# Kernel optimization log

Hardware: AMD Instinct MI355X
Metric: run time of the kernel (lower is better)

The kernel has to match this reference:

```python
import jax, jax.numpy as jnp
import numpy as np

SCALE = 0.125  # 1/sqrt(d_head)
QLEN, KLEN, BSZ, NHEAD, DHEAD = 1024, 1024, 4, 16, 64
RLEN = KLEN + 1


def rel_shift(x, klen):
    # x: [q, r, b, n] -> relative shift -> [q, klen, b, n]
    q, r, b, n = x.shape
    x = x.reshape(r, q, b, n)[1:]
    x = x.reshape(q, r - 1, b, n)[:, :klen]
    return x


def setup_inputs() -> dict:
    key = jax.random.key(0)
    ks = jax.random.split(key, 9)
    q_head = jax.random.normal(ks[0], (QLEN, BSZ, NHEAD, DHEAD), jnp.float32)
    k_head_h = jax.random.normal(ks[1], (KLEN, BSZ, NHEAD, DHEAD), jnp.float32)
    v_head_h = jax.random.normal(ks[2], (KLEN, BSZ, NHEAD, DHEAD), jnp.float32)
    k_head_r = jax.random.normal(ks[3], (RLEN, BSZ, NHEAD, DHEAD), jnp.float32)
    seg_embed = jax.random.normal(ks[4], (2, NHEAD, DHEAD), jnp.float32)
    seg_mat = jax.random.randint(ks[5], (QLEN, KLEN, BSZ), 0, 2) > 0  # bool
    r_w_bias = jax.random.normal(ks[6], (NHEAD, DHEAD), jnp.float32) * 0.02
    r_r_bias = jax.random.normal(ks[7], (NHEAD, DHEAD), jnp.float32) * 0.02
    r_s_bias = jax.random.normal(ks[8], (NHEAD, DHEAD), jnp.float32) * 0.02
    # causal mask: 1.0 where key position j is after query position i
    i = jnp.arange(QLEN)[:, None]
    j = jnp.arange(KLEN)[None, :]
    attn_mask = (j > i).astype(jnp.float32).reshape(QLEN, KLEN, 1, 1)
    return {
        "q_head": q_head, "k_head_h": k_head_h, "v_head_h": v_head_h,
        "k_head_r": k_head_r, "seg_embed": seg_embed, "seg_mat": seg_mat,
        "r_w_bias": r_w_bias, "r_r_bias": r_r_bias, "r_s_bias": r_s_bias,
        "attn_mask": attn_mask,
    }


def reference(q_head, k_head_h, v_head_h, k_head_r, seg_embed, seg_mat,
              r_w_bias, r_r_bias, r_s_bias, attn_mask):
    # content-based score: [q, k, b, n]
    ac = jnp.einsum('ibnd,jbnd->ijbn', q_head + r_w_bias, k_head_h)
    # position-based score, then relative shift
    bd = jnp.einsum('ibnd,jbnd->ijbn', q_head + r_r_bias, k_head_r)
    bd = rel_shift(bd, klen=ac.shape[1])
    # segment-based score: [q, 2, b, n] -> select same/diff per (i,j,b)
    ef = jnp.einsum('ibnd,snd->isbn', q_head + r_s_bias, seg_embed)
    ef = jnp.where(seg_mat[..., None], ef[:, 1:2], ef[:, 0:1])  # [q,k,b,n]
    attn_score = (ac + bd + ef) * SCALE
    attn_score = attn_score - 1e30 * attn_mask
    attn_prob = jax.nn.softmax(attn_score, axis=1)  # softmax over key axis j
    attn_vec = jnp.einsum('ijbn,jbnd->ibnd', attn_prob, v_head_h)
    return attn_vec
```

## Files before the change

### kernel.cpp

```cpp
#include <hip/hip_runtime.h>

#define QLEN  1024
#define KLEN  1024
#define BSZ   4
#define NHEAD 16
#define DHEAD 64
#define PS    4096
#define SCALE 0.125f
#define MSHIFT 16.0f

#define WK 72
#define WR 72
#define WV 68
#define WP 68

typedef __attribute__((ext_vector_type(8))) short  short8;
typedef __attribute__((ext_vector_type(4))) short  short4v;
typedef __attribute__((ext_vector_type(4))) float  float4v;

union S8 { short8 v; short4v h[2]; unsigned short u[8]; };

__device__ __forceinline__ unsigned short f2b(float f) {
    unsigned u; __builtin_memcpy(&u, &f, 4);
    return (unsigned short)((u + 0x8000u) >> 16);
}
__device__ __forceinline__ float b2f(unsigned short s) {
    unsigned u = ((unsigned)s) << 16;
    float f; __builtin_memcpy(&f, &u, 4);
    return f;
}

#define MFMA(a,b,c) __builtin_amdgcn_mfma_f32_16x16x32_bf16((a),(b),(c),0,0,0)

__global__ __launch_bounds__(256)
void seg_pack(const int* __restrict__ sm, unsigned long long* __restrict__ bits)
{
    int gw = (blockIdx.x << 2) + (threadIdx.x >> 6);
    int jw = gw & 15;
    int ib = gw >> 4;
    int b  = ib & 3;
    int i  = ib >> 2;
    int jj = threadIdx.x & 63;
    int v  = sm[(i*KLEN + (jw << 6) + jj)*BSZ + b];
    unsigned long long m = __ballot(v != 0);
    if (jj == 0) bits[gw] = m;
}

__global__ __launch_bounds__(256, 3)
void relattn_mfma7(const float* __restrict__ q,
                   const float* __restrict__ kh,
                   const float* __restrict__ vh,
                   const float* __restrict__ kr,
                   const float* __restrict__ seg_embed,
                   const unsigned long long* __restrict__ segbits,
                   const float* __restrict__ rw,
                   const float* __restrict__ rr,
                   const float* __restrict__ rs,
                   float* __restrict__ out)
{
    __shared__ __align__(16) unsigned short sK [64*WK];
    __shared__ __align__(16) unsigned short sKr[128*WR];
    __shared__ __align__(16) unsigned short sVt[64*WV];
    __shared__ __align__(16) unsigned short sBD[64*WP];

    const int tid  = threadIdx.x;
    const int lane = tid & 63;
    const int wave = tid >> 6;
    const int quad = lane >> 4;
    const int l16  = lane & 15;
    const int bx   = blockIdx.x;
    const int h    = blockIdx.y;
    const int b    = h >> 4;
    const int n    = h & 15;
    const int qt   = (b & 1) ? bx : (15 - bx);
    const int i0   = qt << 6;
    const int m0   = wave << 4;
    const int hoff = h << 6;
    const int d0   = quad << 3;
    const int G0   = 961 - i0;
    const int srow = tid >> 4;
    const int c4   = (tid & 15) << 2;

    float4 pK[4], pV[4], pR[4];
    {
        float4 pR2[4];
        const float4 zf4 = make_float4(0.f, 0.f, 0.f, 0.f);
        #pragma unroll
        for (int k2 = 0; k2 < 4; ++k2) {
            int row = srow + (k2 << 4);
            pK[k2] = *(const float4*)(kh + row*PS + hoff + c4);
            pV[k2] = *(const float4*)(vh + row*PS + hoff + c4);
            int g1 = G0 + row;
            pR[k2]  = (g1 <= 1024) ? *(const float4*)(kr + g1*PS + hoff + c4) : zf4;
            int g2 = G0 + 64 + row;
            pR2[k2] = (g2 <= 1024) ? *(const float4*)(kr + g2*PS + hoff + c4) : zf4;
        }

        float qv[16], rwv[16], rrv[16], rsv[16];
        {
            const float* qp = q + (i0 + m0 + l16)*PS + hoff;
            *(float4*)&qv[0]  = *(const float4*)(qp + d0);
            *(float4*)&qv[4]  = *(const float4*)(qp + d0 + 4);
            *(float4*)&qv[8]  = *(const float4*)(qp + 32 + d0);
            *(float4*)&qv[12] = *(const float4*)(qp + 32 + d0 + 4);
            const float* rwp = rw + n*DHEAD;
            *(float4*)&rwv[0]  = *(const float4*)(rwp + d0);
            *(float4*)&rwv[4]  = *(const float4*)(rwp + d0 + 4);
            *(float4*)&rwv[8]  = *(const float4*)(rwp + 32 + d0);
            *(float4*)&rwv[12] = *(const float4*)(rwp + 32 + d0 + 4);
            const float* rrp = rr + n*DHEAD;
            *(float4*)&rrv[0]  = *(const float4*)(rrp + d0);
            *(float4*)&rrv[4]  = *(const float4*)(rrp + d0 + 4);
            *(float4*)&rrv[8]  = *(const float4*)(rrp + 32 + d0);
            *(float4*)&rrv[12] = *(const float4*)(rrp + 32 + d0 + 4);
            const float* rsp = rs + n*DHEAD;
            *(float4*)&rsv[0]  = *(const float4*)(rsp + d0);
            *(float4*)&rsv[4]  = *(const float4*)(rsp + d0 + 4);
            *(float4*)&rsv[8]  = *(const float4*)(rsp + 32 + d0);
            *(float4*)&rsv[12] = *(const float4*)(rsp + 32 + d0 + 4);
        }
        S8 aw0_, aw1_, ar0_, ar1_;
        #pragma unroll
        for (int m = 0; m < 8; ++m) {
            aw0_.u[m] = f2b(qv[m]   + rwv[m]);
            aw1_.u[m] = f2b(qv[8+m] + rwv[8+m]);
            ar0_.u[m] = f2b(qv[m]   + rrv[m]);
            ar1_.u[m] = f2b(qv[8+m] + rrv[8+m]);
        }
        float ef0r_[4], ef1r_[4];
        {
            const float* se0 = seg_embed + n*DHEAD;
            const float* se1 = seg_embed + (NHEAD + n)*DHEAD;
            float e0 = 0.f, e1 = 0.f;
            #pragma unroll
            for (int m = 0; m < 8; ++m) {
                float qs = qv[m] + rsv[m];
                e0 += qs * se0[d0 + m];  e1 += qs * se1[d0 + m];
                float qs2 = qv[8+m] + rsv[8+m];
                e0 += qs2 * se0[32 + d0 + m];  e1 += qs2 * se1[32 + d0 + m];
            }
            e0 += __shfl_xor(e0, 16); e0 += __shfl_xor(e0, 32);
            e1 += __shfl_xor(e1, 16); e1 += __shfl_xor(e1, 32);
            #pragma unroll
            for (int r = 0; r < 4; ++r) {
                ef0r_[r] = __shfl(e0, (quad << 2) + r);
                ef1r_[r] = __shfl(e1, (quad << 2) + r);
            }
        }

        #pragma unroll
        for (int k2 = 0; k2 < 4; ++k2) {
            int row = srow + (k2 << 4);
            float4 kv = pK[k2];
            short4v kb = {(short)f2b(kv.x),(short)f2b(kv.y),(short)f2b(kv.z),(short)f2b(kv.w)};
            *(short4v*)&sK[row*WK + c4] = kb;
            float4 vv = pV[k2];
            sVt[(c4+0)*WV + row] = f2b(vv.x);
            sVt[(c4+1)*WV + row] = f2b(vv.y);
            sVt[(c4+2)*WV + row] = f2b(vv.z);
            sVt[(c4+3)*WV + row] = f2b(vv.w);
            float4 r1 = pR[k2];
            short4v rb1 = {(short)f2b(r1.x),(short)f2b(r1.y),(short)f2b(r1.z),(short)f2b(r1.w)};
            *(short4v*)&sKr[row*WR + c4] = rb1;
            float4 r2 = pR2[k2];
            short4v rb2 = {(short)f2b(r2.x),(short)f2b(r2.y),(short)f2b(r2.z),(short)f2b(r2.w)};
            *(short4v*)&sKr[(64 + row)*WR + c4] = rb2;
        }

        sK[0] = sK[0];
        __syncthreads();

        #pragma unroll
        for (int m = 0; m < 8; ++m) {  }
        float lp[4];
        float4v Ov[4];
        #pragma unroll
        for (int r = 0; r < 4; ++r) lp[r] = 0.f;
        #pragma unroll
        for (int cb = 0; cb < 4; ++cb) Ov[cb] = (float4v){0.f,0.f,0.f,0.f};

        for (int jt = 0; jt <= qt; ++jt) {
            const int  j0   = jt << 6;
            const bool diag = (jt == qt);
            const bool more = (jt < qt);
            const int  rot  = (jt & 1) << 2;

            if (more) {
                const int j0n = j0 + 64;
                const float4 zf4l = make_float4(0.f, 0.f, 0.f, 0.f);
                #pragma unroll
                for (int k2 = 0; k2 < 4; ++k2) {
                    int row = srow + (k2 << 4);
                    pK[k2] = *(const float4*)(kh + (j0n + row)*PS + hoff + c4);
                    pV[k2] = *(const float4*)(vh + (j0n + row)*PS + hoff + c4);
                    int g = G0 + ((jt + 2) << 6) + row;
                    pR[k2] = (g <= 1024) ? *(const float4*)(kr + g*PS + hoff + c4) : zf4l;
                }
            }
            unsigned long long wbits[4];
            #pragma unroll
            for (int r = 0; r < 4; ++r) {
                int il = m0 + (quad << 2) + r;
                wbits[r] = segbits[(((i0+il) << 2) + b)*16 + jt] >> l16;
            }

            const int bbHi = diag ? wave : 3;
            float4v ac[4];
            #pragma unroll
            for (int bb = 0; bb < 4; ++bb) {
                ac[bb] = (float4v){0.f,0.f,0.f,0.f};
                if (bb <= bbHi) {
                    const unsigned short* kp = &sK[((bb<<4) + l16)*WK + d0];
                    short8 b0 = *(const short8*)kp;
                    short8 b1 = *(const short8*)(kp + 32);
                    ac[bb] = MFMA(aw0_.v, b0, ac[bb]);
                    ac[bb] = MFMA(aw1_.v, b1, ac[bb]);
                }
            }

            const int cbLo = 3 - wave;
            const int cbHi = diag ? 3 : (7 - wave);
            #pragma unroll
            for (int cb = 0; cb < 8; ++cb) {
                if (cb >= cbLo && cb <= cbHi) {
                    const unsigned short* rp = &sKr[((((cb + rot) & 7) << 4) + l16)*WR + d0];
                    short8 b0 = *(const short8*)rp;
                    short8 b1 = *(const short8*)(rp + 32);
                    float4v z = (float4v){0.f,0.f,0.f,0.f};
                    z = MFMA(ar0_.v, b0, z);
                    z = MFMA(ar1_.v, b1, z);
                    #pragma unroll
                    for (int r = 0; r < 4; ++r) {
                        int il = m0 + (quad << 2) + r;
                        int jl = (cb << 4) + l16 - 63 + il;
                        if (jl >= 0 && jl < 64)
                            sBD[il*WP + jl] = f2b(z[r]);
                    }
                }
            }

            #pragma unroll
            for (int r = 0; r < 4; ++r) {
                const int il = m0 + (quad << 2) + r;
                float psum = 0.f;
                #pragma unroll
                for (int bb = 0; bb < 4; ++bb) {
                    const int jl = (bb << 4) + l16;
                    float bd = b2f(sBD[il*WP + jl]);
                    float ef = ((wbits[r] >> (bb << 4)) & 1ull) ? ef1r_[r] : ef0r_[r];
                    float s  = (ac[bb][r] + bd + ef) * SCALE - MSHIFT;
                    if (j0 + jl > i0 + il) s = -1e30f;
                    float p = __expf(s);
                    psum += p;
                    sBD[il*WP + jl] = f2b(p);
                }
                lp[r] += psum;
            }

            {
                const unsigned short* pr = &sBD[(m0 + l16)*WP + d0];
                S8 pa0, pa1;
                pa0.h[0] = *(const short4v*)pr;
                pa0.h[1] = *(const short4v*)(pr + 4);
                pa1.h[0] = *(const short4v*)(pr + 32);
                pa1.h[1] = *(const short4v*)(pr + 36);
                const bool k2on = !(diag && wave < 2);
                #pragma unroll
                for (int cb = 0; cb < 4; ++cb) {
                    const unsigned short* vp = &sVt[((cb<<4) + l16)*WV + d0];
                    S8 v0, v1;
                    v0.h[0] = *(const short4v*)vp;
                    v0.h[1] = *(const short4v*)(vp + 4);
                    Ov[cb] = MFMA(pa0.v, v0.v, Ov[cb]);
                    if (k2on) {
                        v1.h[0] = *(const short4v*)(vp + 32);
                        v1.h[1] = *(const short4v*)(vp + 36);
                        Ov[cb] = MFMA(pa1.v, v1.v, Ov[cb]);
                    }
                }
            }

            if (more) {
                __syncthreads();
                const int krslot = (jt & 1) << 6;
                #pragma unroll
                for (int k2 = 0; k2 < 4; ++k2) {
                    int row = srow + (k2 << 4);
                    float4 kv = pK[k2];
                    short4v kb = {(short)f2b(kv.x),(short)f2b(kv.y),(short)f2b(kv.z),(short)f2b(kv.w)};
                    *(short4v*)&sK[row*WK + c4] = kb;
                    float4 vv = pV[k2];
                    sVt[(c4+0)*WV + row] = f2b(vv.x);
                    sVt[(c4+1)*WV + row] = f2b(vv.y);
                    sVt[(c4+2)*WV + row] = f2b(vv.z);
                    sVt[(c4+3)*WV + row] = f2b(vv.w);
                    float4 rv = pR[k2];
                    short4v rb = {(short)f2b(rv.x),(short)f2b(rv.y),(short)f2b(rv.z),(short)f2b(rv.w)};
                    *(short4v*)&sKr[(krslot + row)*WR + c4] = rb;
                }
                __syncthreads();
            }
        }

        #pragma unroll
        for (int r = 0; r < 4; ++r) {
            float l = lp[r];
            l += __shfl_xor(l, 1);
            l += __shfl_xor(l, 2);
            l += __shfl_xor(l, 4);
            l += __shfl_xor(l, 8);
            const float inv = 1.f / l;
            const int il = m0 + (quad << 2) + r;
            #pragma unroll
            for (int cb = 0; cb < 4; ++cb)
                out[(i0+il)*PS + hoff + (cb<<4) + l16] = Ov[cb][r] * inv;
        }
    }
}

extern "C" void kernel_launch(void* const* d_in, const int* in_sizes, int n_in,
                              void* d_out, int out_size, void* d_ws, size_t ws_size,
                              hipStream_t stream)
{
    const float* q  = (const float*)d_in[0];
    const float* kh = (const float*)d_in[1];
    const float* vh = (const float*)d_in[2];
    const float* kr = (const float*)d_in[3];
    const float* se = (const float*)d_in[4];
    const int*   sm = (const int*)  d_in[5];
    const float* rw = (const float*)d_in[6];
    const float* rr = (const float*)d_in[7];
    const float* rs = (const float*)d_in[8];
    float* o = (float*)d_out;
    unsigned long long* bits = (unsigned long long*)d_ws;
    (void)in_sizes; (void)n_in; (void)out_size; (void)ws_size;

    seg_pack<<<dim3(QLEN*BSZ*16/4), 256, 0, stream>>>(sm, bits);

    dim3 grid(QLEN/64, BSZ*NHEAD);
    relattn_mfma7<<<grid, 256, 0, stream>>>(q, kh, vh, kr, se, bits, rw, rr, rs, o);
}
```

Measured before the change: 287.4 us.

## Swizzle LDS tiles, vectorize seg packing, reorder blocks, raise occupancy

Replaces the padded shared-memory layouts with XOR-swizzled unpadded tiles, which shrinks LDS per block so the launch bound can rise to four blocks per SM while still avoiding bank conflicts. The segment-packing kernel now reads int4 across the batch dimension and emits four ballots per wave, cutting its thread count and load instructions. The attention kernel moves to a 1D grid with a new causal-tile ordering meant to balance long and short query tiles across the machine. It also adds s_setprio around the MFMA sections. Raising the occupancy target may cause register spills.

```diff
diff --git a/kernel.cpp b/kernel.cpp
--- a/kernel.cpp
+++ b/kernel.cpp
@@ -9,11 +9,6 @@
 #define SCALE 0.125f
 #define MSHIFT 16.0f
 
-#define WK 72
-#define WR 72
-#define WV 68
-#define WP 68
-
 typedef __attribute__((ext_vector_type(8))) short  short8;
 typedef __attribute__((ext_vector_type(4))) short  short4v;
 typedef __attribute__((ext_vector_type(4))) float  float4v;
@@ -30,24 +25,31 @@
     return f;
 }
 
+__device__ __forceinline__ int swz (int row, int col) { return (row << 6) + (col ^ (( row        & 7) << 3)); }
+__device__ __forceinline__ int swzV(int row, int col) { return (row << 6) + (col ^ (((row >> 2) & 7) << 3)); }
+
 #define MFMA(a,b,c) __builtin_amdgcn_mfma_f32_16x16x32_bf16((a),(b),(c),0,0,0)
 
 __global__ __launch_bounds__(256)
-void seg_pack(const int* __restrict__ sm, unsigned long long* __restrict__ bits)
+void seg_pack(const int4* __restrict__ sm4, unsigned long long* __restrict__ bits)
 {
-    int gw = (blockIdx.x << 2) + (threadIdx.x >> 6);
-    int jw = gw & 15;
-    int ib = gw >> 4;
-    int b  = ib & 3;
-    int i  = ib >> 2;
+    int w  = (blockIdx.x << 2) + (threadIdx.x >> 6);
+    int i  = w >> 4;
+    int jw = w & 15;
     int jj = threadIdx.x & 63;
-    int v  = sm[(i*KLEN + (jw << 6) + jj)*BSZ + b];
-    unsigned long long m = __ballot(v != 0);
-    if (jj == 0) bits[gw] = m;
-}
-
-__global__ __launch_bounds__(256, 3)
-void relattn_mfma7(const float* __restrict__ q,
+    int4 v = sm4[i*KLEN + (jw << 6) + jj];
+    unsigned long long m0 = __ballot(v.x != 0);
+    unsigned long long m1 = __ballot(v.y != 0);
+    unsigned long long m2 = __ballot(v.z != 0);
+    unsigned long long m3 = __ballot(v.w != 0);
+    if (jj == 0) {
+        unsigned long long* p = bits + (i << 6) + jw;
+        p[0] = m0; p[16] = m1; p[32] = m2; p[48] = m3;
+    }
+}
+
+__global__ __launch_bounds__(256, 4)
+void relattn_mfma8(const float* __restrict__ q,
                    const float* __restrict__ kh,
                    const float* __restrict__ vh,
                    const float* __restrict__ kr,
@@ -58,21 +60,26 @@
                    const float* __restrict__ rs,
                    float* __restrict__ out)
 {
-    __shared__ __align__(16) unsigned short sK [64*WK];
-    __shared__ __align__(16) unsigned short sKr[128*WR];
-    __shared__ __align__(16) unsigned short sVt[64*WV];
-    __shared__ __align__(16) unsigned short sBD[64*WP];
+    __shared__ __align__(16) unsigned short sK [ 64*64];
+    __shared__ __align__(16) unsigned short sKr[128*64];
+    __shared__ __align__(16) unsigned short sVt[ 64*64];
+    __shared__ __align__(16) unsigned short sBD[ 64*64];
 
     const int tid  = threadIdx.x;
     const int lane = tid & 63;
     const int wave = tid >> 6;
     const int quad = lane >> 4;
     const int l16  = lane & 15;
-    const int bx   = blockIdx.x;
-    const int h    = blockIdx.y;
+
+    const int id = blockIdx.x;
+    const int h  = id & 63;
+    const int t  = id >> 6;
+    const int m  = t & 3;
+    const int kq = t >> 2;
+    const int qt = (kq == 0) ? m : (kq == 1) ? (15 - m) : (kq == 2) ? (m + 4) : (11 - m);
+
     const int b    = h >> 4;
     const int n    = h & 15;
-    const int qt   = (b & 1) ? bx : (15 - bx);
     const int i0   = qt << 6;
     const int m0   = wave << 4;
     const int hoff = h << 6;
@@ -81,9 +88,8 @@
     const int srow = tid >> 4;
     const int c4   = (tid & 15) << 2;
 
-    float4 pK[4], pV[4], pR[4];
+    float4 pK[4], pV[4], pR[4], pR2[4];
     {
-        float4 pR2[4];
         const float4 zf4 = make_float4(0.f, 0.f, 0.f, 0.f);
         #pragma unroll
         for (int k2 = 0; k2 < 4; ++k2) {
@@ -95,226 +101,226 @@
             int g2 = G0 + 64 + row;
             pR2[k2] = (g2 <= 1024) ? *(const float4*)(kr + g2*PS + hoff + c4) : zf4;
         }
-
-        float qv[16], rwv[16], rrv[16], rsv[16];
-        {
-            const float* qp = q + (i0 + m0 + l16)*PS + hoff;
-            *(float4*)&qv[0]  = *(const float4*)(qp + d0);
-            *(float4*)&qv[4]  = *(const float4*)(qp + d0 + 4);
-            *(float4*)&qv[8]  = *(const float4*)(qp + 32 + d0);
-            *(float4*)&qv[12] = *(const float4*)(qp + 32 + d0 + 4);
-            const float* rwp = rw + n*DHEAD;
-            *(float4*)&rwv[0]  = *(const float4*)(rwp + d0);
-            *(float4*)&rwv[4]  = *(const float4*)(rwp + d0 + 4);
-            *(float4*)&rwv[8]  = *(const float4*)(rwp + 32 + d0);
-            *(float4*)&rwv[12] = *(const float4*)(rwp + 32 + d0 + 4);
-            const float* rrp = rr + n*DHEAD;
-            *(float4*)&rrv[0]  = *(const float4*)(rrp + d0);
-            *(float4*)&rrv[4]  = *(const float4*)(rrp + d0 + 4);
-            *(float4*)&rrv[8]  = *(const float4*)(rrp + 32 + d0);
-            *(float4*)&rrv[12] = *(const float4*)(rrp + 32 + d0 + 4);
-            const float* rsp = rs + n*DHEAD;
-            *(float4*)&rsv[0]  = *(const float4*)(rsp + d0);
-            *(float4*)&rsv[4]  = *(const float4*)(rsp + d0 + 4);
-            *(float4*)&rsv[8]  = *(const float4*)(rsp + 32 + d0);
-            *(float4*)&rsv[12] = *(const float4*)(rsp + 32 + d0 + 4);
-        }
-        S8 aw0_, aw1_, ar0_, ar1_;
-        #pragma unroll
-        for (int m = 0; m < 8; ++m) {
-            aw0_.u[m] = f2b(qv[m]   + rwv[m]);
-            aw1_.u[m] = f2b(qv[8+m] + rwv[8+m]);
-            ar0_.u[m] = f2b(qv[m]   + rrv[m]);
-            ar1_.u[m] = f2b(qv[8+m] + rrv[8+m]);
-        }
-        float ef0r_[4], ef1r_[4];
-        {
-            const float* se0 = seg_embed + n*DHEAD;
-            const float* se1 = seg_embed + (NHEAD + n)*DHEAD;
-            float e0 = 0.f, e1 = 0.f;
+    }
+
+    float qv[16], rwv[16], rrv[16], rsv[16];
+    {
+        const float* qp = q + (i0 + m0 + l16)*PS + hoff;
+        *(float4*)&qv[0]  = *(const float4*)(qp + d0);
+        *(float4*)&qv[4]  = *(const float4*)(qp + d0 + 4);
+        *(float4*)&qv[8]  = *(const float4*)(qp + 32 + d0);
+        *(float4*)&qv[12] = *(const float4*)(qp + 32 + d0 + 4);
+        const float* rwp = rw + n*DHEAD;
+        *(float4*)&rwv[0]  = *(const float4*)(rwp + d0);
+        *(float4*)&rwv[4]  = *(const float4*)(rwp + d0 + 4);
+        *(float4*)&rwv[8]  = *(const float4*)(rwp + 32 + d0);
+        *(float4*)&rwv[12] = *(const float4*)(rwp + 32 + d0 + 4);
+        const float* rrp = rr + n*DHEAD;
+        *(float4*)&rrv[0]  = *(const float4*)(rrp + d0);
+        *(float4*)&rrv[4]  = *(const float4*)(rrp + d0 + 4);
+        *(float4*)&rrv[8]  = *(const float4*)(rrp + 32 + d0);
+        *(float4*)&rrv[12] = *(const float4*)(rrp + 32 + d0 + 4);
+        const float* rsp = rs + n*DHEAD;
+        *(float4*)&rsv[0]  = *(const float4*)(rsp + d0);
+        *(float4*)&rsv[4]  = *(const float4*)(rsp + d0 + 4);
+        *(float4*)&rsv[8]  = *(const float4*)(rsp + 32 + d0);
+        *(float4*)&rsv[12] = *(const float4*)(rsp + 32 + d0 + 4);
+    }
+    S8 aw0, aw1, ar0, ar1;
+    #pragma unroll
+    for (int mm = 0; mm < 8; ++mm) {
+        aw0.u[mm] = f2b(qv[mm]   + rwv[mm]);
+        aw1.u[mm] = f2b(qv[8+mm] + rwv[8+mm]);
+        ar0.u[mm] = f2b(qv[mm]   + rrv[mm]);
+        ar1.u[mm] = f2b(qv[8+mm] + rrv[8+mm]);
+    }
+    float ef0r[4], ef1r[4];
+    {
+        const float* se0 = seg_embed + n*DHEAD;
+        const float* se1 = seg_embed + (NHEAD + n)*DHEAD;
+        float e0 = 0.f, e1 = 0.f;
+        #pragma unroll
+        for (int mm = 0; mm < 8; ++mm) {
+            float qs = qv[mm] + rsv[mm];
+            e0 += qs * se0[d0 + mm];  e1 += qs * se1[d0 + mm];
+            float qs2 = qv[8+mm] + rsv[8+mm];
+            e0 += qs2 * se0[32 + d0 + mm];  e1 += qs2 * se1[32 + d0 + mm];
+        }
+        e0 += __shfl_xor(e0, 16); e0 += __shfl_xor(e0, 32);
+        e1 += __shfl_xor(e1, 16); e1 += __shfl_xor(e1, 32);
+        #pragma unroll
+        for (int r = 0; r < 4; ++r) {
+            ef0r[r] = __shfl(e0, (quad << 2) + r);
+            ef1r[r] = __shfl(e1, (quad << 2) + r);
+        }
+    }
+
+    #pragma unroll
+    for (int k2 = 0; k2 < 4; ++k2) {
+        int row = srow + (k2 << 4);
+        float4 kv = pK[k2];
+        short4v kb = {(short)f2b(kv.x),(short)f2b(kv.y),(short)f2b(kv.z),(short)f2b(kv.w)};
+        *(short4v*)&sK[swz(row, c4)] = kb;
+        float4 vv = pV[k2];
+        sVt[swzV(c4+0, row)] = f2b(vv.x);
+        sVt[swzV(c4+1, row)] = f2b(vv.y);
+        sVt[swzV(c4+2, row)] = f2b(vv.z);
+        sVt[swzV(c4+3, row)] = f2b(vv.w);
+        float4 r1 = pR[k2];
+        short4v rb1 = {(short)f2b(r1.x),(short)f2b(r1.y),(short)f2b(r1.z),(short)f2b(r1.w)};
+        *(short4v*)&sKr[swz(row, c4)] = rb1;
+        float4 r2 = pR2[k2];
+        short4v rb2 = {(short)f2b(r2.x),(short)f2b(r2.y),(short)f2b(r2.z),(short)f2b(r2.w)};
+        *(short4v*)&sKr[swz(64 + row, c4)] = rb2;
+    }
+    __syncthreads();
+
+    float lp[4];
+    float4v Ov[4];
+    #pragma unroll
+    for (int r = 0; r < 4; ++r) lp[r] = 0.f;
+    #pragma unroll
+    for (int cb = 0; cb < 4; ++cb) Ov[cb] = (float4v){0.f,0.f,0.f,0.f};
+
+    for (int jt = 0; jt <= qt; ++jt) {
+        const int  j0   = jt << 6;
+        const bool diag = (jt == qt);
+        const bool more = (jt < qt);
+        const int  rot  = (jt & 1) << 2;
+
+        if (more) {
+            const int j0n = j0 + 64;
+            const float4 zf4l = make_float4(0.f, 0.f, 0.f, 0.f);
             #pragma unroll
-            for (int m = 0; m < 8; ++m) {
-                float qs = qv[m] + rsv[m];
-                e0 += qs * se0[d0 + m];  e1 += qs * se1[d0 + m];
-                float qs2 = qv[8+m] + rsv[8+m];
-                e0 += qs2 * se0[32 + d0 + m];  e1 += qs2 * se1[32 + d0 + m];
-            }
-            e0 += __shfl_xor(e0, 16); e0 += __shfl_xor(e0, 32);
-            e1 += __shfl_xor(e1, 16); e1 += __shfl_xor(e1, 32);
-            #pragma unroll
-            for (int r = 0; r < 4; ++r) {
-                ef0r_[r] = __shfl(e0, (quad << 2) + r);
-                ef1r_[r] = __shfl(e1, (quad << 2) + r);
-            }
-        }
-
-        #pragma unroll
-        for (int k2 = 0; k2 < 4; ++k2) {
-            int row = srow + (k2 << 4);
-            float4 kv = pK[k2];
-            short4v kb = {(short)f2b(kv.x),(short)f2b(kv.y),(short)f2b(kv.z),(short)f2b(kv.w)};
-            *(short4v*)&sK[row*WK + c4] = kb;
-            float4 vv = pV[k2];
-            sVt[(c4+0)*WV + row] = f2b(vv.x);
-            sVt[(c4+1)*WV + row] = f2b(vv.y);
-            sVt[(c4+2)*WV + row] = f2b(vv.z);
-            sVt[(c4+3)*WV + row] = f2b(vv.w);
-            float4 r1 = pR[k2];
-            short4v rb1 = {(short)f2b(r1.x),(short)f2b(r1.y),(short)f2b(r1.z),(short)f2b(r1.w)};
-            *(short4v*)&sKr[row*WR + c4] = rb1;
-            float4 r2 = pR2[k2];
-            short4v rb2 = {(short)f2b(r2.x),(short)f2b(r2.y),(short)f2b(r2.z),(short)f2b(r2.w)};
-            *(short4v*)&sKr[(64 + row)*WR + c4] = rb2;
-        }
-
-        sK[0] = sK[0];
-        __syncthreads();
-
-        #pragma unroll
-        for (int m = 0; m < 8; ++m) {  }
-        float lp[4];
-        float4v Ov[4];
-        #pragma unroll
-        for (int r = 0; r < 4; ++r) lp[r] = 0.f;
-        #pragma unroll
-        for (int cb = 0; cb < 4; ++cb) Ov[cb] = (float4v){0.f,0.f,0.f,0.f};
-
-        for (int jt = 0; jt <= qt; ++jt) {
-            const int  j0   = jt << 6;
-            const bool diag = (jt == qt);
-            const bool more = (jt < qt);
-            const int  rot  = (jt & 1) << 2;
-
-            if (more) {
-                const int j0n = j0 + 64;
-                const float4 zf4l = make_float4(0.f, 0.f, 0.f, 0.f);
+            for (int k2 = 0; k2 < 4; ++k2) {
+                int row = srow + (k2 << 4);
+                pK[k2] = *(const float4*)(kh + (j0n + row)*PS + hoff + c4);
+                pV[k2] = *(const float4*)(vh + (j0n + row)*PS + hoff + c4);
+                int g = G0 + ((jt + 2) << 6) + row;
+                pR[k2] = (g <= 1024) ? *(const float4*)(kr + g*PS + hoff + c4) : zf4l;
+            }
+        }
+        unsigned long long wbits[4];
+        #pragma unroll
+        for (int r = 0; r < 4; ++r) {
+            int il = m0 + (quad << 2) + r;
+            wbits[r] = segbits[(((i0+il) << 2) + b)*16 + jt] >> l16;
+        }
+
+        __builtin_amdgcn_s_setprio(1);
+        const int bbHi = diag ? wave : 3;
+        float4v ac[4];
+        #pragma unroll
+        for (int bb = 0; bb < 4; ++bb) {
+            ac[bb] = (float4v){0.f,0.f,0.f,0.f};
+            if (bb <= bbHi) {
+                const int krow = (bb << 4) + l16;
+                short8 b0 = *(const short8*)&sK[swz(krow, d0)];
+                short8 b1 = *(const short8*)&sK[swz(krow, d0 + 32)];
+                ac[bb] = MFMA(aw0.v, b0, ac[bb]);
+                ac[bb] = MFMA(aw1.v, b1, ac[bb]);
+            }
+        }
+
+        const int cbLo = 3 - wave;
+        const int cbHi = diag ? 3 : (7 - wave);
+        #pragma unroll
+        for (int cb = 0; cb < 8; ++cb) {
+            if (cb >= cbLo && cb <= cbHi) {
+                const int rrow = (((cb + rot) & 7) << 4) + l16;
+                short8 b0 = *(const short8*)&sKr[swz(rrow, d0)];
+                short8 b1 = *(const short8*)&sKr[swz(rrow, d0 + 32)];
+                float4v z = (float4v){0.f,0.f,0.f,0.f};
+                z = MFMA(ar0.v, b0, z);
+                z = MFMA(ar1.v, b1, z);
                 #pragma unroll
-                for (int k2 = 0; k2 < 4; ++k2) {
-                    int row = srow + (k2 << 4);
-                    pK[k2] = *(const float4*)(kh + (j0n + row)*PS + hoff + c4);
-                    pV[k2] = *(const float4*)(vh + (j0n + row)*PS + hoff + c4);
-                    int g = G0 + ((jt + 2) << 6) + row;
-                    pR[k2] = (g <= 1024) ? *(const float4*)(kr + g*PS + hoff + c4) : zf4l;
+                for (int r = 0; r < 4; ++r) {
+                    int il = m0 + (quad << 2) + r;
+                    int jl = (cb << 4) + l16 - 63 + il;
+                    if (jl >= 0 && jl < 64)
+                        sBD[swz(il, jl)] = f2b(z[r]);
                 }
             }
-            unsigned long long wbits[4];
-            #pragma unroll
-            for (int r = 0; r < 4; ++r) {
-                int il = m0 + (quad << 2) + r;
-                wbits[r] = segbits[(((i0+il) << 2) + b)*16 + jt] >> l16;
-            }
-
-            const int bbHi = diag ? wave : 3;
-            float4v ac[4];
+        }
+        __builtin_amdgcn_s_setprio(0);
+
+        #pragma unroll
+        for (int r = 0; r < 4; ++r) {
+            const int il = m0 + (quad << 2) + r;
+            float psum = 0.f;
             #pragma unroll
             for (int bb = 0; bb < 4; ++bb) {
-                ac[bb] = (float4v){0.f,0.f,0.f,0.f};
-                if (bb <= bbHi) {
-                    const unsigned short* kp = &sK[((bb<<4) + l16)*WK + d0];
-                    short8 b0 = *(const short8*)kp;
-                    short8 b1 = *(const short8*)(kp + 32);
-                    ac[bb] = MFMA(aw0_.v, b0, ac[bb]);
-                    ac[bb] = MFMA(aw1_.v, b1, ac[bb]);
+                const int jl = (bb << 4) + l16;
+                float bd = b2f(sBD[swz(il, jl)]);
+                float ef = ((wbits[r] >> (bb << 4)) & 1ull) ? ef1r[r] : ef0r[r];
+                float s  = (ac[bb][r] + bd + ef) * SCALE - MSHIFT;
+                if (j0 + jl > i0 + il) s = -1e30f;
+                float p = __expf(s);
+                psum += p;
+                sBD[swz(il, jl)] = f2b(p);
+            }
+            lp[r] += psum;
+        }
+
+        {
+            const int prow = m0 + l16;
+            S8 pa0, pa1;
+            pa0.h[0] = *(const short4v*)&sBD[swz(prow, d0)];
+            pa0.h[1] = *(const short4v*)&sBD[swz(prow, d0 + 4)];
+            pa1.h[0] = *(const short4v*)&sBD[swz(prow, d0 + 32)];
+            pa1.h[1] = *(const short4v*)&sBD[swz(prow, d0 + 36)];
+            const bool k2on = !(diag && wave < 2);
+            __builtin_amdgcn_s_setprio(1);
+            #pragma unroll
+            for (int cb = 0; cb < 4; ++cb) {
+                const int vrow = (cb << 4) + l16;
+                S8 v0, v1;
+                v0.h[0] = *(const short4v*)&sVt[swzV(vrow, d0)];
+                v0.h[1] = *(const short4v*)&sVt[swzV(vrow, d0 + 4)];
+                Ov[cb] = MFMA(pa0.v, v0.v, Ov[cb]);
+                if (k2on) {
+                    v1.h[0] = *(const short4v*)&sVt[swzV(vrow, d0 + 32)];
+                    v1.h[1] = *(const short4v*)&sVt[swzV(vrow, d0 + 36)];
+                    Ov[cb] = MFMA(pa1.v, v1.v, Ov[cb]);
                 }
             }
-
-            const int cbLo = 3 - wave;
-            const int cbHi = diag ? 3 : (7 - wave);
+            __builtin_amdgcn_s_setprio(0);
+        }
+
+        if (more) {
+            __syncthreads();
+            const int krslot = (jt & 1) << 6;
             #pragma unroll
-            for (int cb = 0; cb < 8; ++cb) {
-                if (cb >= cbLo && cb <= cbHi) {
-                    const unsigned short* rp = &sKr[((((cb + rot) & 7) << 4) + l16)*WR + d0];
-                    short8 b0 = *(const short8*)rp;
-                    short8 b1 = *(const short8*)(rp + 32);
-                    float4v z = (float4v){0.f,0.f,0.f,0.f};
-                    z = MFMA(ar0_.v, b0, z);
-                    z = MFMA(ar1_.v, b1, z);
-                    #pragma unroll
-                    for (int r = 0; r < 4; ++r) {
-                        int il = m0 + (quad << 2) + r;
-                        int jl = (cb << 4) + l16 - 63 + il;
-                        if (jl >= 0 && jl < 64)
-                            sBD[il*WP + jl] = f2b(z[r]);
-                    }
-                }
-            }
-
-            #pragma unroll
-            for (int r = 0; r < 4; ++r) {
-                const int il = m0 + (quad << 2) + r;
-                float psum = 0.f;
-                #pragma unroll
-                for (int bb = 0; bb < 4; ++bb) {
-                    const int jl = (bb << 4) + l16;
-                    float bd = b2f(sBD[il*WP + jl]);
-                    float ef = ((wbits[r] >> (bb << 4)) & 1ull) ? ef1r_[r] : ef0r_[r];
-                    float s  = (ac[bb][r] + bd + ef) * SCALE - MSHIFT;
-                    if (j0 + jl > i0 + il) s = -1e30f;
-                    float p = __expf(s);
-                    psum += p;
-                    sBD[il*WP + jl] = f2b(p);
-                }
-                lp[r] += psum;
-            }
-
-            {
-                const unsigned short* pr = &sBD[(m0 + l16)*WP + d0];
-                S8 pa0, pa1;
-                pa0.h[0] = *(const short4v*)pr;
-                pa0.h[1] = *(const short4v*)(pr + 4);
-                pa1.h[0] = *(const short4v*)(pr + 32);
-                pa1.h[1] = *(const short4v*)(pr + 36);
-                const bool k2on = !(diag && wave < 2);
-                #pragma unroll
-                for (int cb = 0; cb < 4; ++cb) {
-                    const unsigned short* vp = &sVt[((cb<<4) + l16)*WV + d0];
-                    S8 v0, v1;
-                    v0.h[0] = *(const short4v*)vp;
-                    v0.h[1] = *(const short4v*)(vp + 4);
-                    Ov[cb] = MFMA(pa0.v, v0.v, Ov[cb]);
-                    if (k2on) {
-                        v1.h[0] = *(const short4v*)(vp + 32);
-                        v1.h[1] = *(const short4v*)(vp + 36);
-                        Ov[cb] = MFMA(pa1.v, v1.v, Ov[cb]);
-                    }
-                }
-            }
-
-            if (more) {
-                __syncthreads();
-                const int krslot = (jt & 1) << 6;
-                #pragma unroll
-                for (int k2 = 0; k2 < 4; ++k2) {
-                    int row = srow + (k2 << 4);
-                    float4 kv = pK[k2];
-                    short4v kb = {(short)f2b(kv.x),(short)f2b(kv.y),(short)f2b(kv.z),(short)f2b(kv.w)};
-                    *(short4v*)&sK[row*WK + c4] = kb;
-                    float4 vv = pV[k2];
-                    sVt[(c4+0)*WV + row] = f2b(vv.x);
-                    sVt[(c4+1)*WV + row] = f2b(vv.y);
-                    sVt[(c4+2)*WV + row] = f2b(vv.z);
-                    sVt[(c4+3)*WV + row] = f2b(vv.w);
-                    float4 rv = pR[k2];
-                    short4v rb = {(short)f2b(rv.x),(short)f2b(rv.y),(short)f2b(rv.z),(short)f2b(rv.w)};
-                    *(short4v*)&sKr[(krslot + row)*WR + c4] = rb;
-                }
-                __syncthreads();
-            }
-        }
-
-        #pragma unroll
-        for (int r = 0; r < 4; ++r) {
-            float l = lp[r];
-            l += __shfl_xor(l, 1);
-            l += __shfl_xor(l, 2);
-            l += __shfl_xor(l, 4);
-            l += __shfl_xor(l, 8);
-            const float inv = 1.f / l;
-            const int il = m0 + (quad << 2) + r;
-            #pragma unroll
-            for (int cb = 0; cb < 4; ++cb)
-                out[(i0+il)*PS + hoff + (cb<<4) + l16] = Ov[cb][r] * inv;
-        }
+            for (int k2 = 0; k2 < 4; ++k2) {
+                int row = srow + (k2 << 4);
+                float4 kv = pK[k2];
+                short4v kb = {(short)f2b(kv.x),(short)f2b(kv.y),(short)f2b(kv.z),(short)f2b(kv.w)};
+                *(short4v*)&sK[swz(row, c4)] = kb;
+                float4 vv = pV[k2];
+                sVt[swzV(c4+0, row)] = f2b(vv.x);
+                sVt[swzV(c4+1, row)] = f2b(vv.y);
+                sVt[swzV(c4+2, row)] = f2b(vv.z);
+                sVt[swzV(c4+3, row)] = f2b(vv.w);
+                float4 rv = pR[k2];
+                short4v rb = {(short)f2b(rv.x),(short)f2b(rv.y),(short)f2b(rv.z),(short)f2b(rv.w)};
+                *(short4v*)&sKr[swz(krslot + row, c4)] = rb;
+            }
+            __syncthreads();
+        }
+    }
+
+    #pragma unroll
+    for (int r = 0; r < 4; ++r) {
+        float l = lp[r];
+        l += __shfl_xor(l, 1);
+        l += __shfl_xor(l, 2);
+        l += __shfl_xor(l, 4);
+        l += __shfl_xor(l, 8);
+        const float inv = 1.f / l;
+        const int il = m0 + (quad << 2) + r;
+        #pragma unroll
+        for (int cb = 0; cb < 4; ++cb)
+            out[(i0+il)*PS + hoff + (cb<<4) + l16] = Ov[cb][r] * inv;
     }
 }
 
@@ -335,8 +341,7 @@
     unsigned long long* bits = (unsigned long long*)d_ws;
     (void)in_sizes; (void)n_in; (void)out_size; (void)ws_size;
 
-    seg_pack<<<dim3(QLEN*BSZ*16/4), 256, 0, stream>>>(sm, bits);
-
-    dim3 grid(QLEN/64, BSZ*NHEAD);
-    relattn_mfma7<<<grid, 256, 0, stream>>>(q, kh, vh, kr, se, bits, rw, rr, rs, o);
-}
+    seg_pack<<<dim3(QLEN*16/4), 256, 0, stream>>>((const int4*)sm, bits);
+
+    relattn_mfma8<<<dim3(QLEN/64 * BSZ * NHEAD), 256, 0, stream>>>(q, kh, vh, kr, se, bits, rw, rr, rs, o);
+}
```

Result: slower. 505.4 us (+75.8%).
